# Kernel tuning notes

Measured on AMD Instinct MI355X. Metric: run time of the kernel, lower is better.

## Reference

```python
import jax, jax.numpy as jnp
import numpy as np

BATCH, SEQ, EMBED = 8, 1024, 2048
HEADS, LATENT = 16, 512
HEAD_DIM = EMBED // HEADS            # 128
NOPE = HEAD_DIM // 4                 # 32 (qk_rope_dim=96 is even, no adjust)
ROPE_D = HEAD_DIM - NOPE             # 96
THETA = 10000.0


def _rope_tables(seq_len):
    # matches torch: freqs over arange(0, rope_dim, 2)/rope_dim
    freqs = 1.0 / THETA ** (jnp.arange(0, ROPE_D, 2, dtype=jnp.float32) / ROPE_D)
    emb = jnp.arange(seq_len, dtype=jnp.float32)[:, None] * freqs[None, :]  # [S, ROPE_D//2]
    return jnp.cos(emb), jnp.sin(emb)


def _apply_rope(x, cos, sin):
    # x: [B,H,S,D]; cos/sin: [S,D//2]. NOTE: original concatenates halves (non-interleaved output).
    xe, xo = x[..., ::2], x[..., 1::2]
    return jnp.concatenate([xe * cos - xo * sin, xo * cos + xe * sin], axis=-1)


def setup_inputs() -> dict:
    key = jax.random.key(0)
    ks = jax.random.split(key, 5)
    x = jax.random.normal(ks[0], (BATCH, SEQ, EMBED), jnp.float32)
    Wq = jax.random.normal(ks[1], (EMBED, EMBED), jnp.float32) * 0.02
    Wkv_down = jax.random.normal(ks[2], (EMBED, LATENT), jnp.float32) * 0.02
    Wk_up = jax.random.normal(ks[3], (LATENT, EMBED), jnp.float32) * 0.02
    Wv_up = jax.random.normal(ks[4], (LATENT, EMBED), jnp.float32) * 0.02
    return {"x": x, "Wq": Wq, "Wkv_down": Wkv_down, "Wk_up": Wk_up, "Wv_up": Wv_up}


def reference(x, Wq, Wkv_down, Wk_up, Wv_up):
    B, S, E = x.shape
    # projections (weights stored [in, out], equivalent to nn.Linear math)
    q = (x @ Wq).reshape(B, S, HEADS, HEAD_DIM).transpose(0, 2, 1, 3)   # [B,H,S,D]
    q_nope, q_rope = q[..., :NOPE], q[..., NOPE:]
    c_kv = x @ Wkv_down                                                  # [B,S,latent]
    k = (c_kv @ Wk_up).reshape(B, S, HEADS, HEAD_DIM).transpose(0, 2, 1, 3)
    v = (c_kv @ Wv_up).reshape(B, S, HEADS, HEAD_DIM).transpose(0, 2, 1, 3)
    k_nope, k_rope = k[..., :NOPE], k[..., NOPE:]

    cos, sin = _rope_tables(S)
    q_rope = _apply_rope(q_rope, cos, sin)
    k_rope = _apply_rope(k_rope, cos, sin)

    qf = jnp.concatenate([q_nope, q_rope], axis=-1)
    kf = jnp.concatenate([k_nope, k_rope], axis=-1)

    scale = jnp.float32(1.0 / np.sqrt(HEAD_DIM))
    scores = jnp.einsum('bhqd,bhkd->bhqk', qf, kf) * scale
    causal = jnp.triu(jnp.ones((S, S), dtype=bool), k=1)  # past_length=0
    scores = jnp.where(causal, -jnp.inf, scores)
    weights = jax.nn.softmax(scores, axis=-1)
    out = jnp.einsum('bhqk,bhkd->bhqd', weights, v)
    return out.transpose(0, 2, 1, 3).reshape(B, S, E)
```

## Files before the change

### kernel.cpp

```cpp
#include <hip/hip_runtime.h>
#include <stdint.h>

typedef unsigned short u16;
typedef __bf16 bf16x8 __attribute__((ext_vector_type(8)));
typedef float    f32x4 __attribute__((ext_vector_type(4)));
typedef unsigned short u16x8 __attribute__((ext_vector_type(8)));
typedef unsigned short u16x4 __attribute__((ext_vector_type(4)));

#define BB 8
#define SS 1024
#define EE 2048
#define HH 16
#define DD 128

__device__ __forceinline__ u16 f2bf(float f){
  union { float f; unsigned u; } v; v.f = f;
  unsigned r = v.u + 0x7FFFu + ((v.u >> 16) & 1u);
  return (u16)(r >> 16);
}
__device__ __forceinline__ float bf2f(u16 h){
  union { unsigned u; float f; } v; v.u = ((unsigned)h) << 16;
  return v.f;
}
__device__ __forceinline__ bf16x8 ld8(const u16* p){
  return __builtin_bit_cast(bf16x8, *(const u16x8*)p);
}

typedef __attribute__((address_space(1))) const unsigned int gas_u32;
typedef __attribute__((address_space(3))) unsigned int las_u32;
__device__ __forceinline__ void g2l16(const u16* g, u16* l){
  __builtin_amdgcn_global_load_lds((gas_u32*)g, (las_u32*)l, 16, 0, 0);
}

#define BARRIER() asm volatile("s_barrier" ::: "memory")
#define VMC(n)    asm volatile("s_waitcnt vmcnt(" #n ")" ::: "memory")

__global__ __launch_bounds__(256) void cvt_f32_bf16(const float* __restrict__ in,
                                                    u16* __restrict__ out, int n){
  int i = (blockIdx.x*256 + threadIdx.x)*8;
  if (i >= n) return;
  float4 v0 = *(const float4*)(in + i);
  float4 v1 = *(const float4*)(in + i + 4);
  u16x8 o;
  o[0]=f2bf(v0.x); o[1]=f2bf(v0.y); o[2]=f2bf(v0.z); o[3]=f2bf(v0.w);
  o[4]=f2bf(v1.x); o[5]=f2bf(v1.y); o[6]=f2bf(v1.z); o[7]=f2bf(v1.w);
  *(u16x8*)(out + i) = o;
}

__global__ __launch_bounds__(256) void transposeW(const float* __restrict__ W,
                                                  u16* __restrict__ Wt, int K, int N){
  __shared__ float t[32][33];
  int c = threadIdx.x & 31, r = threadIdx.x >> 5;
  int bx = blockIdx.x, by = blockIdx.y;
  #pragma unroll
  for (int i = 0; i < 32; i += 8)
    t[r+i][c] = W[(size_t)(by*32 + r + i)*N + bx*32 + c];
  __syncthreads();
  #pragma unroll
  for (int i = 0; i < 32; i += 8)
    Wt[(size_t)(bx*32 + r + i)*K + by*32 + c] = f2bf(t[c][r+i]);
}

__global__ __launch_bounds__(256) void rope_tables(float* __restrict__ cosb,
                                                   float* __restrict__ sinb){
  int i = blockIdx.x*256 + threadIdx.x;
  if (i >= SS*48) return;
  int s = i / 48, j = i % 48;
  float freq = powf(10000.0f, -((float)(2*j)) / 96.0f);
  float e = (float)s * freq;
  cosb[i] = cosf(e);
  sinb[i] = sinf(e);
}

__global__ __launch_bounds__(256) void rope_apply2(u16* __restrict__ qp,
                                                   u16* __restrict__ kp,
                                                   const float* __restrict__ cosb,
                                                   const float* __restrict__ sinb){
  u16* base = blockIdx.y ? kp : qp;
  int t = blockIdx.x*256 + threadIdx.x;
  int row = t >> 4, h = t & 15, s = row & (SS-1);
  u16* p = base + (size_t)row*EE + h*DD + 32;
  float e[48], o[48];
  #pragma unroll
  for (int c = 0; c < 12; c++){
    u16x8 v = *(const u16x8*)(p + c*8);
    #pragma unroll
    for (int j = 0; j < 4; j++){
      e[c*4 + j] = bf2f(v[2*j]);
      o[c*4 + j] = bf2f(v[2*j+1]);
    }
  }
  u16 ob[96];
  #pragma unroll
  for (int j = 0; j < 48; j++){
    float cs = cosb[s*48 + j], sn = sinb[s*48 + j];
    ob[j]      = f2bf(e[j]*cs - o[j]*sn);
    ob[48 + j] = f2bf(o[j]*cs + e[j]*sn);
  }
  #pragma unroll
  for (int c = 0; c < 12; c++)
    *(u16x8*)(p + c*8) = *(const u16x8*)(ob + c*8);
}

__global__ __launch_bounds__(256) void gemm_bt(const u16* __restrict__ A,
    const u16* __restrict__ Bt, u16* __restrict__ C, int M, int N, int K){
  __shared__ u16 Al[128*32];
  __shared__ u16 Bl[128*32];
  const int tid = threadIdx.x;
  const int lane = tid & 63, w = tid >> 6;
  const int wr = w >> 1, wc = w & 1;
  const int l15 = lane & 15, l4 = lane >> 4;
  const int bm = blockIdx.y*128, bn = blockIdx.x*128;
  const int srow = tid >> 2;
  const int skc  = (tid & 3) * 8;
  const u16* ga = A  + (size_t)(bm + srow)*K + skc;
  const u16* gb = Bt + (size_t)(bn + srow)*K + skc;
  u16* la = Al + w*512;
  u16* lb = Bl + w*512;
  f32x4 acc[4][4] = {};
  for (int k0 = 0; k0 < K; k0 += 32){
    __syncthreads();
    g2l16(ga + k0,          la);
    g2l16(ga + 64*K + k0,   la + 2048);
    g2l16(gb + k0,          lb);
    g2l16(gb + 64*K + k0,   lb + 2048);
    __syncthreads();
    bf16x8 af[4], bfr[4];
    #pragma unroll
    for (int m = 0; m < 4; m++) af[m]  = ld8(Al + (wr*64 + m*16 + l15)*32 + l4*8);
    #pragma unroll
    for (int n = 0; n < 4; n++) bfr[n] = ld8(Bl + (wc*64 + n*16 + l15)*32 + l4*8);
    #pragma unroll
    for (int m = 0; m < 4; m++)
      #pragma unroll
      for (int n = 0; n < 4; n++)
        acc[m][n] = __builtin_amdgcn_mfma_f32_16x16x32_bf16(af[m], bfr[n], acc[m][n], 0, 0, 0);
  }
  #pragma unroll
  for (int m = 0; m < 4; m++)
    #pragma unroll
    for (int n = 0; n < 4; n++)
      #pragma unroll
      for (int r = 0; r < 4; r++){
        int row = bm + wr*64 + m*16 + l4*4 + r;
        int col = bn + wc*64 + n*16 + l15;
        C[(size_t)row*N + col] = f2bf(acc[m][n][r]);
      }
}

#define AFR(ab, mf, ks) ld8(&AL[ab][wr][((mf)*16 + l15)*64 + ((((ks)*4 + l4) ^ r7) << 3)])
#define BFR(bb, nf, ks) ld8(&BL[bb][wc>>1][(((wc&1)*64 + (nf)*16 + l15))*64 + ((((ks)*4 + l4) ^ r7) << 3)])

#define STAGE_A(ab, h, kt) stage2(aRow, (h), (kt), K, &AL[ab][h][0], wj0)
#define STAGE_A2(ab, kt)   do{ STAGE_A(ab, 0, kt); STAGE_A(ab, 1, kt); }while(0)
#define STAGE_B(bb, h, kt) stage2(bRow, (h), (kt), K, &BL[bb][h][0], wj0)

__device__ __forceinline__ void stage2(const u16* rowbase, int h, int kt, int K,
                                       u16* lds, int wj0){
  const u16* g = rowbase + (size_t)h*128*K + kt*64;
  g2l16(g,               lds + wj0*512);
  g2l16(g + (size_t)8*K, lds + wj0*512 + 512);
}

#define PHASE(ab, q, LOADB, STAGE, DOVM) do{                                       \
  bf16x8 a00 = AFR(ab, 2*(q)  , 0);                                               \
  bf16x8 a01 = AFR(ab, 2*(q)  , 1);                                               \
  bf16x8 a10 = AFR(ab, 2*(q)+1, 0);                                               \
  bf16x8 a11 = AFR(ab, 2*(q)+1, 1);                                               \
  if (LOADB){                                                                      \
    _Pragma("unroll")                                                              \
    for (int nf = 0; nf < 4; nf++){ bq[nf][0]=BFR(ab,nf,0); bq[nf][1]=BFR(ab,nf,1); } \
  }                                                                                \
  STAGE;                                                                           \
  if (DOVM) VMC(4);                                                                \
  BARRIER();                                                                       \
  __builtin_amdgcn_s_setprio(1);                                                   \
  _Pragma("unroll")                                                                \
  for (int nf = 0; nf < 4; nf++){                                                  \
    acc[2*(q)][nf]   = __builtin_amdgcn_mfma_f32_16x16x32_bf16(a00, bq[nf][0], acc[2*(q)][nf],0,0,0);   \
    acc[2*(q)+1][nf] = __builtin_amdgcn_mfma_f32_16x16x32_bf16(a10, bq[nf][0], acc[2*(q)+1][nf],0,0,0); \
  }                                                                                \
  _Pragma("unroll")                                                                \
  for (int nf = 0; nf < 4; nf++){                                                  \
    acc[2*(q)][nf]   = __builtin_amdgcn_mfma_f32_16x16x32_bf16(a01, bq[nf][1], acc[2*(q)][nf],0,0,0);   \
    acc[2*(q)+1][nf] = __builtin_amdgcn_mfma_f32_16x16x32_bf16(a11, bq[nf][1], acc[2*(q)+1][nf],0,0,0); \
  }                                                                                \
  __builtin_amdgcn_s_setprio(0);                                                   \
  BARRIER();                                                                       \
  __builtin_amdgcn_sched_barrier(0);                                               \
}while(0)

__global__ __launch_bounds__(512, 2) void gemm8(const u16* __restrict__ A,
    const u16* __restrict__ Bt, u16* __restrict__ C0, u16* __restrict__ C1,
    int K, int Nout0, int Nout1, int nsplit, int vt){
  __shared__ u16 AL[2][2][128*64];
  __shared__ u16 BL[2][2][128*64];
  const int tid = threadIdx.x, lane = tid & 63, w = tid >> 6;
  const int wr = w >> 2, wc = w & 3;
  const int l15 = lane & 15, l4 = lane >> 4;
  const int r7 = l15 & 7;
  const int bm = blockIdx.y*256, bn = blockIdx.x*256;
  const int wj0 = w*2;
  const int cswz = (lane & 7) ^ (lane >> 3);
  const u16* aRow = A  + (size_t)(bm + wj0*8 + (lane>>3))*K + cswz*8;
  const u16* bRow = Bt + (size_t)(bn + wj0*8 + (lane>>3))*K + cswz*8;

  const int nkt = K >> 6;
  const int niter = nkt >> 1;

  STAGE_A2(0, 0);
  STAGE_B(0, 0, 0); STAGE_B(0, 1, 0);
  STAGE_B(1, 0, 1); STAGE_B(1, 1, 1);
  VMC(4);
  BARRIER();

  f32x4 acc[8][4] = {};
  bf16x8 bq[4][2];

  for (int it = 0; it < niter; ++it){
    const int kt1 = 2*it + 1;
    int kt2 = 2*it + 2; if (kt2 >= nkt) kt2 -= nkt;
    int kt3 = 2*it + 3; if (kt3 >= nkt) kt3 -= nkt;
    PHASE(0, 0, 1, STAGE_A2(1, kt1),    0);
    PHASE(0, 1, 0, STAGE_B(0, 0, kt2),  0);
    PHASE(0, 2, 0, STAGE_B(0, 1, kt2),  0);
    PHASE(0, 3, 0, ;,                   1);
    PHASE(1, 0, 1, STAGE_A2(0, kt2),    0);
    PHASE(1, 1, 0, STAGE_B(1, 0, kt3),  0);
    PHASE(1, 2, 0, STAGE_B(1, 1, kt3),  0);
    PHASE(1, 3, 0, ;,                   1);
  }
  asm volatile("s_waitcnt vmcnt(0)" ::: "memory");

  if (vt && bn >= nsplit){
    const int bcol = bn - nsplit;
    #pragma unroll
    for (int mf = 0; mf < 8; mf++)
      #pragma unroll
      for (int nf = 0; nf < 4; nf++){
        int row0 = bm + wr*128 + mf*16 + l4*4;
        int col  = bcol + wc*64 + nf*16 + l15;
        int bh = (row0 >> 10)*16 + (col >> 7);
        int d  = col & 127;
        int s  = row0 & 1023;
        u16x4 pk;
        #pragma unroll
        for (int r = 0; r < 4; r++) pk[r] = f2bf(acc[mf][nf][r]);
        *(u16x4*)(C1 + (((size_t)(bh*128 + d)) << 10) + s) = pk;
      }
  } else {
    u16* Cd = (bn < nsplit) ? C0 : C1;
    const int No = (bn < nsplit) ? Nout0 : Nout1;
    const int bcol = (bn < nsplit) ? bn : bn - nsplit;
    #pragma unroll
    for (int mf = 0; mf < 8; mf++)
      #pragma unroll
      for (int nf = 0; nf < 4; nf++)
        #pragma unroll
        for (int r = 0; r < 4; r++){
          int row = bm + wr*128 + mf*16 + l4*4 + r;
          int col = bcol + wc*64 + nf*16 + l15;
          Cd[(size_t)row*No + col] = f2bf(acc[mf][nf][r]);
        }
  }
}

#define PLW 40

__global__ __launch_bounds__(512) void attn(const u16* __restrict__ qp,
                                            const u16* __restrict__ kp,
                                            const u16* __restrict__ vpT,
                                            float* __restrict__ out){
  __shared__ u16 Kl[2][64*128];
  __shared__ u16 Vl[2][128*64];
  __shared__ u16 Pl[8][16*PLW];
  const int tid = threadIdx.x, lane = tid & 63, w = tid >> 6;
  const int l15 = lane & 15, l4 = lane >> 4;
  const int qt = 7 - blockIdx.y;
  const int bh = blockIdx.x;
  const int b = bh >> 4, h = bh & 15;
  const int qbase = qt*128;
  const int qmin = qbase + w*16;
  const int qg = qmin + l15;
  const float c = 0.12751920700948998f;
  const float THR = 62.7f;

  const size_t rowq = (size_t)(b*SS + qg)*EE + h*DD;
  bf16x8 qf[4];
  #pragma unroll
  for (int kk = 0; kk < 4; kk++) qf[kk] = ld8(qp + rowq + kk*32 + l4*8);
  #pragma unroll
  for (int kk = 0; kk < 4; kk++) asm volatile("" : "+v"(qf[kk]));

  f32x4 ao[8] = {};
  float mi = -3e38f, li = 0.0f;

  const int ntiles = 2*qt + 2;
  const int vcc = lane & 7;

  #pragma unroll
  for (int q = 0; q < 2; q++){
    int r = w*8 + q*4 + (lane>>4);
    g2l16(kp + (size_t)(b*SS + r)*EE + h*DD + (((lane&15) ^ (r&7))<<3),
          &Kl[0][0] + w*1024 + q*512);
    int d = w*16 + q*8 + (lane>>3);
    g2l16(vpT + (size_t)(bh*DD + d)*SS + ((vcc ^ (d&7))<<3),
          &Vl[0][0] + w*1024 + q*512);
  }

  for (int t = 0; t < ntiles; t++){
    const int kv0 = t*64;
    const int buf = t & 1;
    {
      const int kvn = (t + 1 < ntiles) ? kv0 + 64 : kv0;
      #pragma unroll
      for (int q = 0; q < 2; q++){
        int r = w*8 + q*4 + (lane>>4);
        g2l16(kp + (size_t)(b*SS + kvn + r)*EE + h*DD + (((lane&15) ^ (r&7))<<3),
              &Kl[buf^1][0] + w*1024 + q*512);
        int d = w*16 + q*8 + (lane>>3);
        g2l16(vpT + (size_t)(bh*DD + d)*SS + kvn + ((vcc ^ (d&7))<<3),
              &Vl[buf^1][0] + w*1024 + q*512);
      }
    }
    VMC(4);
    BARRIER();

    if (kv0 <= qmin + 15){
      float sv[4][4];
      __builtin_amdgcn_s_setprio(1);
      #pragma unroll
      for (int nt = 0; nt < 4; nt++){
        f32x4 sacc = {};
        #pragma unroll
        for (int kk = 0; kk < 4; kk++){
          bf16x8 kf = ld8(&Kl[buf][0] + (nt*16 + l15)*128 + (((kk*4 + l4) ^ (l15&7))<<3));
          sacc = __builtin_amdgcn_mfma_f32_16x16x32_bf16(kf, qf[kk], sacc, 0, 0, 0);
        }
        #pragma unroll
        for (int r = 0; r < 4; r++) sv[nt][r] = sacc[r];
      }
      __builtin_amdgcn_s_setprio(0);
      if (kv0 + 63 > qmin){
        #pragma unroll
        for (int nt = 0; nt < 4; nt++)
          #pragma unroll
          for (int r = 0; r < 4; r++){
            int kg = kv0 + nt*16 + l4*4 + r;
            if (kg > qg) sv[nt][r] = -3e38f;
          }
      }
      float mx = sv[0][0];
      #pragma unroll
      for (int nt = 0; nt < 4; nt++)
        #pragma unroll
        for (int r = 0; r < 4; r++) mx = fmaxf(mx, sv[nt][r]);
      mx = fmaxf(mx, __shfl_xor(mx, 16));
      mx = fmaxf(mx, __shfl_xor(mx, 32));
      if (__any(mx > mi + THR)){
        float mnew = fmaxf(mi, mx);
        float alpha = __builtin_amdgcn_exp2f((mi - mnew)*c);
        li *= alpha;
        #pragma unroll
        for (int n8 = 0; n8 < 8; n8++) ao[n8] *= alpha;
        mi = mnew;
      }
      const float mnc = mi*c;
      float pout[4][4];
      float rs = 0.0f;
      #pragma unroll
      for (int nt = 0; nt < 4; nt++)
        #pragma unroll
        for (int r = 0; r < 4; r++){
          float pv = __builtin_amdgcn_exp2f(__builtin_fmaf(sv[nt][r], c, -mnc));
          pout[nt][r] = pv; rs += pv;
        }
      rs += __shfl_xor(rs, 16);
      rs += __shfl_xor(rs, 32);
      li += rs;
      #pragma unroll
      for (int kk = 0; kk < 2; kk++){
        #pragma unroll
        for (int ntl = 0; ntl < 2; ntl++){
          int nt = kk*2 + ntl;
          u16x4 pk;
          #pragma unroll
          for (int r = 0; r < 4; r++) pk[r] = f2bf(pout[nt][r]);
          *(u16x4*)(&Pl[w][l15*PLW + ntl*16 + l4*4]) = pk;
        }
        bf16x8 pa = ld8(&Pl[w][l15*PLW + l4*8]);
        __builtin_amdgcn_s_setprio(1);
        #pragma unroll
        for (int n8 = 0; n8 < 8; n8++){
          bf16x8 vf = ld8(&Vl[buf][0] + (n8*16 + l15)*64 + (((kk*4 + l4) ^ (l15&7))<<3));
          ao[n8] = __builtin_amdgcn_mfma_f32_16x16x32_bf16(vf, pa, ao[n8], 0, 0, 0);
        }
        __builtin_amdgcn_s_setprio(0);
      }
    }
    BARRIER();
  }
  asm volatile("s_waitcnt vmcnt(0)" ::: "memory");

  const float inv = 1.0f / li;
  const size_t orow = (size_t)(b*SS + qg)*EE + h*DD;
  #pragma unroll
  for (int n8 = 0; n8 < 8; n8++){
    f32x4 o = ao[n8]*inv;
    *(float4*)(out + orow + n8*16 + l4*4) = __builtin_bit_cast(float4, o);
  }
}

extern "C" void kernel_launch(void* const* d_in, const int* in_sizes, int n_in,
                              void* d_out, int out_size, void* d_ws, size_t ws_size,
                              hipStream_t stream){
  const float* x    = (const float*)d_in[0];
  const float* Wq   = (const float*)d_in[1];
  const float* Wkvd = (const float*)d_in[2];
  const float* Wku  = (const float*)d_in[3];
  const float* Wvu  = (const float*)d_in[4];
  float* out = (float*)d_out;
  char* ws = (char*)d_ws;

  u16*   xb    = (u16*)  (ws);
  u16*   WqT   = (u16*)  (ws +  33554432);
  u16*   WkvdT = (u16*)  (ws +  41943040);
  u16*   WkuT  = (u16*)  (ws +  44040192);
  u16*   WvuT  = (u16*)  (ws +  46137344);
  float* cosb  = (float*)(ws +  48234496);
  float* sinb  = (float*)(ws +  48431104);
  u16*   qp    = (u16*)  (ws +  48627712);
  u16*   ckv   = (u16*)  (ws +  82182144);
  u16*   kp    = (u16*)  (ws +  90570752);
  u16*   vpT   = (u16*)  (ws + 124125184);

  cvt_f32_bf16<<<(BB*SS*EE)/(256*8), 256, 0, stream>>>(x, xb, BB*SS*EE);
  transposeW<<<dim3(EE/32,  EE/32), 256, 0, stream>>>(Wq,   WqT,   EE,  EE);
  transposeW<<<dim3(512/32, EE/32), 256, 0, stream>>>(Wkvd, WkvdT, EE,  512);
  transposeW<<<dim3(EE/32, 512/32), 256, 0, stream>>>(Wku,  WkuT,  512, EE);
  transposeW<<<dim3(EE/32, 512/32), 256, 0, stream>>>(Wvu,  WvuT,  512, EE);
  rope_tables<<<(SS*48 + 255)/256, 256, 0, stream>>>(cosb, sinb);

  gemm8<<<dim3(EE/256, (BB*SS)/256), 512, 0, stream>>>(xb, WqT, qp, qp,
                                                       EE, EE, EE, EE, 0);
  gemm_bt<<<dim3(512/128, (BB*SS)/128), 256, 0, stream>>>(xb, WkvdT, ckv, BB*SS, 512, EE);
  gemm8<<<dim3(4096/256, (BB*SS)/256), 512, 0, stream>>>(ckv, WkuT, kp, vpT,
                                                         512, EE, 0, EE, 1);

  rope_apply2<<<dim3((BB*SS*HH)/256, 2), 256, 0, stream>>>(qp, kp, cosb, sinb);

  attn<<<dim3(BB*HH, SS/128), 512, 0, stream>>>(qp, kp, vpT, out);
}
```

Baseline: 306.6 us.

## Merge prep kernels into one launch and remap GEMM blocks per XCD

Six preprocessing kernels (input bf16 conversion, four weight transposes, rope table build) are folded into a single launch whose blocks branch on block index, cutting launch overhead and tail gaps between small kernels. Both GEMM kernels also remap the linear block id so that blocks landing on the same XCD (id mod 8) handle neighbouring row tiles. This is meant to improve L2 reuse of A rows within each XCD. The remap assumes the grid row count divides by 8 and the column count is a power of two.

After: 286.4 us. -6.6%, faster.

```diff
diff --git a/kernel.cpp b/kernel.cpp
--- a/kernel.cpp
+++ b/kernel.cpp
@@ -35,23 +35,10 @@
 #define BARRIER() asm volatile("s_barrier" ::: "memory")
 #define VMC(n)    asm volatile("s_waitcnt vmcnt(" #n ")" ::: "memory")
 
-__global__ __launch_bounds__(256) void cvt_f32_bf16(const float* __restrict__ in,
-                                                    u16* __restrict__ out, int n){
-  int i = (blockIdx.x*256 + threadIdx.x)*8;
-  if (i >= n) return;
-  float4 v0 = *(const float4*)(in + i);
-  float4 v1 = *(const float4*)(in + i + 4);
-  u16x8 o;
-  o[0]=f2bf(v0.x); o[1]=f2bf(v0.y); o[2]=f2bf(v0.z); o[3]=f2bf(v0.w);
-  o[4]=f2bf(v1.x); o[5]=f2bf(v1.y); o[6]=f2bf(v1.z); o[7]=f2bf(v1.w);
-  *(u16x8*)(out + i) = o;
-}
-
-__global__ __launch_bounds__(256) void transposeW(const float* __restrict__ W,
-                                                  u16* __restrict__ Wt, int K, int N){
-  __shared__ float t[32][33];
-  int c = threadIdx.x & 31, r = threadIdx.x >> 5;
-  int bx = blockIdx.x, by = blockIdx.y;
+__device__ __forceinline__ void trB(const float* __restrict__ W, u16* __restrict__ Wt,
+                                    int K, int N, int bx, int by,
+                                    float (*t)[33], int tid){
+  int c = tid & 31, r = tid >> 5;
   #pragma unroll
   for (int i = 0; i < 32; i += 8)
     t[r+i][c] = W[(size_t)(by*32 + r + i)*N + bx*32 + c];
@@ -61,15 +48,40 @@
     Wt[(size_t)(bx*32 + r + i)*K + by*32 + c] = f2bf(t[c][r+i]);
 }
 
-__global__ __launch_bounds__(256) void rope_tables(float* __restrict__ cosb,
-                                                   float* __restrict__ sinb){
-  int i = blockIdx.x*256 + threadIdx.x;
-  if (i >= SS*48) return;
-  int s = i / 48, j = i % 48;
-  float freq = powf(10000.0f, -((float)(2*j)) / 96.0f);
-  float e = (float)s * freq;
-  cosb[i] = cosf(e);
-  sinb[i] = sinf(e);
+__global__ __launch_bounds__(256) void prep(const float* __restrict__ x, u16* __restrict__ xb,
+    const float* __restrict__ Wq,   u16* __restrict__ WqT,
+    const float* __restrict__ Wkvd, u16* __restrict__ WkvdT,
+    const float* __restrict__ Wku,  u16* __restrict__ WkuT,
+    const float* __restrict__ Wvu,  u16* __restrict__ WvuT,
+    float* __restrict__ cosb, float* __restrict__ sinb){
+  __shared__ float t[32][33];
+  const int bid = blockIdx.x, tid = threadIdx.x;
+  if (bid < 8192){
+    int i = (bid*256 + tid)*8;
+    float4 v0 = *(const float4*)(x + i);
+    float4 v1 = *(const float4*)(x + i + 4);
+    u16x8 o;
+    o[0]=f2bf(v0.x); o[1]=f2bf(v0.y); o[2]=f2bf(v0.z); o[3]=f2bf(v0.w);
+    o[4]=f2bf(v1.x); o[5]=f2bf(v1.y); o[6]=f2bf(v1.z); o[7]=f2bf(v1.w);
+    *(u16x8*)(xb + i) = o;
+  } else if (bid < 12288){
+    int k = bid - 8192;  trB(Wq,   WqT,   EE,  EE,  k & 63, k >> 6, t, tid);
+  } else if (bid < 13312){
+    int k = bid - 12288; trB(Wkvd, WkvdT, EE,  512, k & 15, k >> 4, t, tid);
+  } else if (bid < 14336){
+    int k = bid - 13312; trB(Wku,  WkuT,  512, EE,  k & 63, k >> 6, t, tid);
+  } else if (bid < 15360){
+    int k = bid - 14336; trB(Wvu,  WvuT,  512, EE,  k & 63, k >> 6, t, tid);
+  } else {
+    int i = (bid - 15360)*256 + tid;
+    if (i < SS*48){
+      int s = i / 48, j = i % 48;
+      float freq = powf(10000.0f, -((float)(2*j)) / 96.0f);
+      float e = (float)s * freq;
+      cosb[i] = cosf(e);
+      sinb[i] = sinf(e);
+    }
+  }
 }
 
 __global__ __launch_bounds__(256) void rope_apply2(u16* __restrict__ qp,
@@ -110,7 +122,10 @@
   const int lane = tid & 63, w = tid >> 6;
   const int wr = w >> 1, wc = w & 1;
   const int l15 = lane & 15, l4 = lane >> 4;
-  const int bm = blockIdx.y*128, bn = blockIdx.x*128;
+  const int id = blockIdx.y * 4 + blockIdx.x;
+  const int xcd = id & 7, j = id >> 3;
+  const int bm = (xcd*8 + (j >> 2)) * 128;
+  const int bn = (j & 3) * 128;
   const int srow = tid >> 2;
   const int skc  = (tid & 3) * 8;
   const u16* ga = A  + (size_t)(bm + srow)*K + skc;
@@ -199,7 +214,13 @@
   const int wr = w >> 2, wc = w & 3;
   const int l15 = lane & 15, l4 = lane >> 4;
   const int r7 = l15 & 7;
-  const int bm = blockIdx.y*256, bn = blockIdx.x*256;
+  const int nbx = gridDim.x;
+  const int lb  = __popc(nbx - 1);
+  const int id  = blockIdx.y * nbx + blockIdx.x;
+  const int xcd = id & 7, j = id >> 3;
+  const int rpx = gridDim.y >> 3;
+  const int bm  = (xcd*rpx + (j >> lb)) * 256;
+  const int bn  = (j & (nbx - 1)) * 256;
   const int wj0 = w*2;
   const int cswz = (lane & 7) ^ (lane >> 3);
   const u16* aRow = A  + (size_t)(bm + wj0*8 + (lane>>3))*K + cswz*8;
@@ -434,12 +455,8 @@
   u16*   kp    = (u16*)  (ws +  90570752);
   u16*   vpT   = (u16*)  (ws + 124125184);
 
-  cvt_f32_bf16<<<(BB*SS*EE)/(256*8), 256, 0, stream>>>(x, xb, BB*SS*EE);
-  transposeW<<<dim3(EE/32,  EE/32), 256, 0, stream>>>(Wq,   WqT,   EE,  EE);
-  transposeW<<<dim3(512/32, EE/32), 256, 0, stream>>>(Wkvd, WkvdT, EE,  512);
-  transposeW<<<dim3(EE/32, 512/32), 256, 0, stream>>>(Wku,  WkuT,  512, EE);
-  transposeW<<<dim3(EE/32, 512/32), 256, 0, stream>>>(Wvu,  WvuT,  512, EE);
-  rope_tables<<<(SS*48 + 255)/256, 256, 0, stream>>>(cosb, sinb);
+  prep<<<15552, 256, 0, stream>>>(x, xb, Wq, WqT, Wkvd, WkvdT,
+                                  Wku, WkuT, Wvu, WvuT, cosb, sinb);
 
   gemm8<<<dim3(EE/256, (BB*SS)/256), 512, 0, stream>>>(xb, WqT, qp, qp,
                                                        EE, EE, EE, EE, 0);
```
